# Performance work log

Measured on AMD Instinct MI355X. Metric: run time of the kernel, lower is better.

Reference implementation:

```python
import math
import jax, jax.numpy as jnp
import numpy as np

B, L, C, H = 8, 1024, 1024, 16
D = C // H  # head_dim = 64
MAX_SCALE_MUL = math.log(100.0)


def setup_inputs() -> dict:
    key = jax.random.key(0)
    ks = jax.random.split(key, 8)
    x = jax.random.normal(ks[0], (B, L, C), dtype=jnp.float32)
    # rotary frequencies: angle(l, j) = l * theta^(-2j/D), stored as (cos, sin)
    theta = 10000.0
    inv_freq = theta ** (-jnp.arange(0, D, 2, dtype=jnp.float32) / D)  # [D/2]
    ang = jnp.arange(L, dtype=jnp.float32)[:, None] * inv_freq[None, :]  # [L, D/2]
    freqs_cis = jnp.stack([jnp.cos(ang), jnp.sin(ang)], axis=-1)  # [L, D/2, 2]
    attn_bias = jnp.zeros((1, 1, L, L), dtype=jnp.float32)
    W_qkv = jax.random.normal(ks[1], (3 * C, C), dtype=jnp.float32) * (1.0 / math.sqrt(C))
    q_bias = jnp.zeros((C,), dtype=jnp.float32)
    v_bias = jnp.zeros((C,), dtype=jnp.float32)
    scale_mul_log = jnp.full((1, H, 1, 1), math.log(4.0), dtype=jnp.float32)
    W_proj = jax.random.normal(ks[2], (C, C), dtype=jnp.float32) * (1.0 / math.sqrt(C))
    b_proj = jnp.zeros((C,), dtype=jnp.float32)
    return {"x": x, "freqs_cis": freqs_cis, "attn_bias": attn_bias,
            "W_qkv": W_qkv, "q_bias": q_bias, "v_bias": v_bias,
            "scale_mul_log": scale_mul_log, "W_proj": W_proj, "b_proj": b_proj}


def _l2norm(t):
    # F.normalize(t, dim=-1): t / max(||t||_2, eps)
    n = jnp.sqrt(jnp.sum(t * t, axis=-1, keepdims=True))
    return t / jnp.maximum(n, 1e-12)


def _rope(t, fr):
    # t: [B,H,L,D]; fr: [L,D/2,2] (cos,sin). Complex mul on adjacent pairs.
    b, h, l, d = t.shape
    t2 = t.reshape(b, h, l, d // 2, 2)
    c = fr[None, None, :, :, 0]
    s = fr[None, None, :, :, 1]
    re = t2[..., 0] * c - t2[..., 1] * s
    im = t2[..., 0] * s + t2[..., 1] * c
    return jnp.stack([re, im], axis=-1).reshape(b, h, l, d)


def reference(x, freqs_cis, attn_bias, W_qkv, q_bias, v_bias, scale_mul_log, W_proj, b_proj):
    b, l, c = x.shape
    bias = jnp.concatenate([q_bias, jnp.zeros_like(q_bias), v_bias])  # [3C]
    qkv = (x @ W_qkv.T + bias).reshape(b, l, 3, H, D)
    # permute(2,0,3,1,4) -> q,k,v each [B,H,L,D]
    q = jnp.transpose(qkv[:, :, 0], (0, 2, 1, 3))
    k = jnp.transpose(qkv[:, :, 1], (0, 2, 1, 3))
    v = jnp.transpose(qkv[:, :, 2], (0, 2, 1, 3))
    # attn_l2_norm path: learned per-head scale, softmax scale = 1
    scale_mul = jnp.exp(jnp.minimum(scale_mul_log, MAX_SCALE_MUL))  # [1,H,1,1]
    q = _l2norm(q) * scale_mul
    k = _l2norm(k)
    q = _rope(q, freqs_cis)
    k = _rope(k, freqs_cis)
    scores = jnp.einsum('bhqd,bhkd->bhqk', q, k) * 1.0 + attn_bias
    attn = jax.nn.softmax(scores, axis=-1)
    out = jnp.einsum('bhqk,bhkd->bhqd', attn, v)
    out = jnp.transpose(out, (0, 2, 1, 3)).reshape(b, l, c)
    return out @ W_proj.T + b_proj
```

## Files before the change

kernel.cpp:

```cpp
#include <hip/hip_runtime.h>
#include <math.h>
#include <type_traits>

#define PB 8
#define PL 1024
#define PC 1024
#define PH 16
#define PD 64
#define MAX_SCALE_MUL 4.605170185988092f
#define LOG2E 1.4426950408889634f

typedef __attribute__((ext_vector_type(8))) short s16x8;
typedef __attribute__((ext_vector_type(4))) float f32x4;

#define MFMA16(a, b, c) __builtin_amdgcn_mfma_f32_16x16x32_bf16(a, b, c, 0, 0, 0)

#if __has_builtin(__builtin_amdgcn_exp2f)
#define EXP2(x) __builtin_amdgcn_exp2f(x)
#else
#define EXP2(x) exp2f(x)
#endif

__device__ __forceinline__ unsigned short f2bf(float f) {
    unsigned u = __float_as_uint(f);
    unsigned r = (u + 0x7fffu + ((u >> 16) & 1u)) >> 16;
    return (unsigned short)r;
}

__device__ __forceinline__ unsigned pk2bf(float a, float b) {
#if __has_builtin(__builtin_amdgcn_cvt_pk_bf16_f32)
    typedef __attribute__((ext_vector_type(2))) __bf16 bf16x2_t;
    bf16x2_t r = __builtin_amdgcn_cvt_pk_bf16_f32(a, b);
    return __builtin_bit_cast(unsigned, r);
#else
    return (unsigned)f2bf(a) | ((unsigned)f2bf(b) << 16);
#endif
}

__device__ __forceinline__ void gl2lds16(const void* g, void* l) {
    __builtin_amdgcn_global_load_lds(
        (const __attribute__((address_space(1))) unsigned int*)g,
        (__attribute__((address_space(3))) unsigned int*)l, 16, 0, 0);
}

__global__ __launch_bounds__(256) void cast3f_kernel(
    const float* __restrict__ a, const float* __restrict__ b,
    const float* __restrict__ c, const float* __restrict__ bias,
    unsigned short* __restrict__ oa, unsigned short* __restrict__ ob,
    unsigned short* __restrict__ oc, int* __restrict__ flag)
{
    int blk = blockIdx.x;
    if (blk >= 12288) {
        int idx = (blk - 12288) * 256 + threadIdx.x;
        const float4* b4 = (const float4*)bias;
        bool nz = false;
#pragma unroll
        for (int i = 0; i < 4; i++) {
            float4 v = b4[idx * 4 + i];
            nz |= (v.x != 0.f) | (v.y != 0.f) | (v.z != 0.f) | (v.w != 0.f);
        }
        if (nz) atomicOr(flag, 1);
        return;
    }
    const float* src; unsigned short* dst; int base;
    if (blk < 8192)       { src = a; dst = oa; base = blk; }
    else if (blk < 11264) { src = b; dst = ob; base = blk - 8192; }
    else                  { src = c; dst = oc; base = blk - 11264; }
    int i = base * 256 + threadIdx.x;
    float4 v = ((const float4*)src)[i];
    ((uint2*)dst)[i] = make_uint2(pk2bf(v.x, v.y), pk2bf(v.z, v.w));
}

__global__ __launch_bounds__(256) void gemm_qkv_lean(
    const unsigned short* __restrict__ Xh,
    const unsigned short* __restrict__ Wh,
    const float* __restrict__ qb, const float* __restrict__ vb,
    const float* __restrict__ freqs,
    unsigned short* __restrict__ Qh, unsigned short* __restrict__ Kh,
    unsigned short* __restrict__ Vt)
{
    __shared__ unsigned short As[128 * 64];
    __shared__ unsigned short Bs[128 * 64];
    const int tid  = threadIdx.x;
    const int wave = tid >> 6, lane = tid & 63;
    const int wm = wave & 1, wn = wave >> 1;
    const int quad = lane >> 4, rr = lane & 15;
    const int m0 = blockIdx.x * 128;
    const int n0 = blockIdx.y * 128;
    const bool vmode = (n0 >= 2048);

    f32x4 acc[4][4];
#pragma unroll
    for (int i = 0; i < 4; i++)
#pragma unroll
        for (int j = 0; j < 4; j++) acc[i][j] = (f32x4){0.f, 0.f, 0.f, 0.f};

    const int r8 = lane >> 3;
    const int c8 = lane & 7;
    const int g  = c8 ^ r8;
    const unsigned short* gA = Xh + (size_t)(m0 + wave * 32 + r8) * 1024 + g * 8;
    const unsigned short* gB = Wh + (size_t)(n0 + wave * 32 + r8) * 1024 + g * 8;
    unsigned short* lA = &As[(wave * 32) * 64];
    unsigned short* lB = &Bs[(wave * 32) * 64];

    const int swz8 = rr & 7;

    auto kloop = [&](auto vm) {
        constexpr int VM = decltype(vm)::value;
        for (int k0 = 0; k0 < 16; k0++) {
#pragma unroll
            for (int t = 0; t < 4; t++) {
                gl2lds16(gA + (size_t)t * 8192, &lA[(t * 8) * 64]);
                gl2lds16(gB + (size_t)t * 8192, &lB[(t * 8) * 64]);
            }
            gA += 64; gB += 64;
            __syncthreads();

#pragma unroll
            for (int kk = 0; kk < 2; kk++) {
                const int coff = ((kk * 4 + quad) ^ swz8) * 8;
                s16x8 wf[4], xf[4];
#pragma unroll
                for (int i = 0; i < 4; i++)
                    wf[i] = *(const s16x8*)&Bs[(wn * 64 + i * 16 + rr) * 64 + coff];
#pragma unroll
                for (int j = 0; j < 4; j++)
                    xf[j] = *(const s16x8*)&As[(wm * 64 + j * 16 + rr) * 64 + coff];
                if constexpr (VM == 0) {
#pragma unroll
                    for (int i = 0; i < 4; i++)
#pragma unroll
                        for (int j = 0; j < 4; j++)
                            acc[i][j] = MFMA16(wf[i], xf[j], acc[i][j]);
                } else {
#pragma unroll
                    for (int i = 0; i < 4; i++)
#pragma unroll
                        for (int j = 0; j < 4; j++)
                            acc[i][j] = MFMA16(xf[j], wf[i], acc[i][j]);
                }
            }
            __syncthreads();
        }
    };
    if (vmode) kloop(std::integral_constant<int, 1>{});
    else       kloop(std::integral_constant<int, 0>{});

    const int b   = m0 >> 10;
    const int h   = ((n0 & 1023) + wn * 64) >> 6;
    const int lb0 = (m0 & 1023) + wm * 64;

    if (vmode) {
        unsigned short* basep = Vt + (size_t)(b * PH + h) * PD * PL;
#pragma unroll
        for (int i = 0; i < 4; i++) {
            const int d = i * 16 + rr;
            const float bv = vb[h * 64 + d];
#pragma unroll
            for (int j = 0; j < 4; j++) {
                const int l0 = lb0 + j * 16 + quad * 4;
                uint2 pk = make_uint2(pk2bf(acc[i][j][0] + bv, acc[i][j][1] + bv),
                                      pk2bf(acc[i][j][2] + bv, acc[i][j][3] + bv));
                *(uint2*)(basep + (size_t)d * PL + l0) = pk;
            }
        }
    } else {
        const int which = n0 >> 10;
        if (which == 0) {
            unsigned short* basep = Qh + (size_t)(b * PH + h) * PL * PD;
#pragma unroll
            for (int i = 0; i < 4; i++) {
                const int d0 = i * 16 + quad * 4;
                const float4 b4 = *(const float4*)(qb + h * 64 + d0);
#pragma unroll
                for (int j = 0; j < 4; j++) {
                    const int l = lb0 + j * 16 + rr;
                    uint2 pk = make_uint2(
                        pk2bf(acc[i][j][0] + b4.x, acc[i][j][1] + b4.y),
                        pk2bf(acc[i][j][2] + b4.z, acc[i][j][3] + b4.w));
                    *(uint2*)(basep + (size_t)l * PD + d0) = pk;
                }
            }
        } else {
            unsigned short* basep = Kh + (size_t)(b * PH + h) * PL * PD;
            const float2* fr2 = (const float2*)freqs;
#pragma unroll
            for (int j = 0; j < 4; j++) {
                float ss = 0.f;
#pragma unroll
                for (int i = 0; i < 4; i++)
                    ss = fmaf(acc[i][j][0], acc[i][j][0],
                         fmaf(acc[i][j][1], acc[i][j][1],
                         fmaf(acc[i][j][2], acc[i][j][2],
                         fmaf(acc[i][j][3], acc[i][j][3], ss))));
                ss += __shfl_xor(ss, 16);
                ss += __shfl_xor(ss, 32);
                const float scale = 1.0f / fmaxf(sqrtf(ss), 1e-12f);
                const int l = lb0 + j * 16 + rr;
#pragma unroll
                for (int i = 0; i < 4; i++) {
                    const int d0 = i * 16 + quad * 4;
                    const float2 cs0 = fr2[(size_t)l * 32 + (d0 >> 1)];
                    const float2 cs1 = fr2[(size_t)l * 32 + (d0 >> 1) + 1];
                    const float a0 = acc[i][j][0] * scale, a1 = acc[i][j][1] * scale;
                    const float a2 = acc[i][j][2] * scale, a3 = acc[i][j][3] * scale;
                    uint2 pk = make_uint2(
                        pk2bf(a0 * cs0.x - a1 * cs0.y, fmaf(a0, cs0.y, a1 * cs0.x)),
                        pk2bf(a2 * cs1.x - a3 * cs1.y, fmaf(a2, cs1.y, a3 * cs1.x)));
                    *(uint2*)(basep + (size_t)l * PD + d0) = pk;
                }
            }
        }
    }
}

__global__ __launch_bounds__(256, 4) void attn_mfma(
    const unsigned short* __restrict__ Qh, const unsigned short* __restrict__ Kh,
    const unsigned short* __restrict__ Vt, const float* __restrict__ bias,
    const float* __restrict__ sml, const int* __restrict__ biasflag,
    const float* __restrict__ freqs, unsigned short* __restrict__ O)
{
    __shared__ unsigned short Ks[2][64 * 64];
    __shared__ unsigned short Vs[2][64 * 64];
    __shared__ unsigned int   Ps[4][16 * 32];

    const int tid  = threadIdx.x;
    const int wave = tid >> 6, lane = tid & 63;
    const int quad = lane >> 4, rr = lane & 15;
    const int bh = blockIdx.x, q0 = blockIdx.y * 128;
    const int b = bh >> 4, h = bh & 15;
    const int hasbias = *biasflag;

    const float M = __expf(fminf(sml[h], MAX_SCALE_MUL)) * LOG2E;
    const f32x4 negM = (f32x4){-M, -M, -M, -M};

    const int sr = wave * 16 + (lane >> 3);
    const int sc = lane & 7;
    const int sg = sc ^ (sr & 7);
    const int swz8 = rr & 7;
    const int psw  = (rr & 7) << 2;

    const size_t kvbase = (size_t)bh * PL * PD;
    const float2* fr2 = (const float2*)freqs;

    auto stage = [&](int buf, int kb) {
        gl2lds16(Kh + kvbase + (size_t)(kb * 64 + sr) * PD + sg * 8,
                 &Ks[buf][(wave * 16) * 64]);
        gl2lds16(Kh + kvbase + (size_t)(kb * 64 + sr + 8) * PD + sg * 8,
                 &Ks[buf][(wave * 16 + 8) * 64]);
        gl2lds16(Vt + kvbase + (size_t)sr * PL + kb * 64 + sg * 8,
                 &Vs[buf][(wave * 16) * 64]);
        gl2lds16(Vt + kvbase + (size_t)(sr + 8) * PL + kb * 64 + sg * 8,
                 &Vs[buf][(wave * 16 + 8) * 64]);
    };

    stage(0, 0);

    s16x8 qB[2][2];
#pragma unroll
    for (int g = 0; g < 2; g++) {
        const int ql = q0 + g * 64 + wave * 16 + rr;
        const size_t qoff = ((size_t)bh * PL + ql) * PD;
        uint4 r0 = *(const uint4*)(Qh + qoff + quad * 8);
        uint4 r1 = *(const uint4*)(Qh + qoff + 32 + quad * 8);
        unsigned uu[8] = {r0.x, r0.y, r0.z, r0.w, r1.x, r1.y, r1.z, r1.w};
        float ss = 0.f;
#pragma unroll
        for (int m = 0; m < 8; m++) {
            float lo = __uint_as_float(uu[m] << 16);
            float hi = __uint_as_float(uu[m] & 0xffff0000u);
            ss = fmaf(lo, lo, fmaf(hi, hi, ss));
        }
        ss += __shfl_xor(ss, 16);
        ss += __shfl_xor(ss, 32);
        const float scale = M / fmaxf(sqrtf(ss), 1e-12f);
        unsigned outw[8];
#pragma unroll
        for (int m = 0; m < 8; m++) {
            const int idx = (m >> 2) * 16 + quad * 4 + (m & 3);
            float2 cs = fr2[(size_t)ql * 32 + idx];
            float lo = __uint_as_float(uu[m] << 16);
            float hi = __uint_as_float(uu[m] & 0xffff0000u);
            float av = lo * scale, bv = hi * scale;
            outw[m] = pk2bf(av * cs.x - bv * cs.y, fmaf(av, cs.y, bv * cs.x));
        }
        qB[g][0] = __builtin_bit_cast(s16x8, make_uint4(outw[0], outw[1], outw[2], outw[3]));
        qB[g][1] = __builtin_bit_cast(s16x8, make_uint4(outw[4], outw[5], outw[6], outw[7]));
    }

    f32x4 accO[2][4];
#pragma unroll
    for (int g = 0; g < 2; g++)
#pragma unroll
        for (int jd = 0; jd < 4; jd++) accO[g][jd] = (f32x4){0.f, 0.f, 0.f, 0.f};
    float lsum[2] = {0.f, 0.f};

    __syncthreads();

    auto kbloop = [&](auto hb) {
        constexpr int HB = decltype(hb)::value;
        int cur = 0;
        for (int kb = 0; kb < 16; kb++) {
            if (kb < 15) stage(cur ^ 1, kb + 1);

            unsigned ps[2][4][2];
#pragma unroll
            for (int s = 0; s < 4; s++) {
                const s16x8 k0 = *(const s16x8*)&Ks[cur][(s * 16 + rr) * 64 + ((0 + quad) ^ swz8) * 8];
                const s16x8 k1 = *(const s16x8*)&Ks[cur][(s * 16 + rr) * 64 + ((4 + quad) ^ swz8) * 8];
#pragma unroll
                for (int g = 0; g < 2; g++) {
                    __builtin_amdgcn_s_setprio(1);
                    f32x4 z = MFMA16(k0, qB[g][0], negM);
                    z = MFMA16(k1, qB[g][1], z);
                    __builtin_amdgcn_s_setprio(0);
                    if constexpr (HB) {
                        const float* brow = bias + (size_t)(q0 + g * 64 + wave * 16 + rr) * PL + kb * 64;
                        float4 bv = *(const float4*)(brow + s * 16 + quad * 4);
                        z[0] = fmaf(bv.x, LOG2E, z[0]);
                        z[1] = fmaf(bv.y, LOG2E, z[1]);
                        z[2] = fmaf(bv.z, LOG2E, z[2]);
                        z[3] = fmaf(bv.w, LOG2E, z[3]);
                    }
                    z[0] = EXP2(z[0]); z[1] = EXP2(z[1]);
                    z[2] = EXP2(z[2]); z[3] = EXP2(z[3]);
                    lsum[g] += (z[0] + z[1]) + (z[2] + z[3]);
                    ps[g][s][0] = pk2bf(z[0], z[1]);
                    ps[g][s][1] = pk2bf(z[2], z[3]);
                }
            }

            s16x8 pB[2][2];
#pragma unroll
            for (int g = 0; g < 2; g++) {
#pragma unroll
                for (int s = 0; s < 4; s++)
                    *(uint2*)&Ps[wave][rr * 32 + ((s * 8 + quad * 2) ^ psw)] =
                        make_uint2(ps[g][s][0], ps[g][s][1]);
                pB[g][0] = *(const s16x8*)&Ps[wave][rr * 32 + ((quad * 4) ^ psw)];
                pB[g][1] = *(const s16x8*)&Ps[wave][rr * 32 + ((16 + quad * 4) ^ psw)];
            }
#pragma unroll
            for (int jd = 0; jd < 4; jd++) {
                const s16x8 v0 = *(const s16x8*)&Vs[cur][(jd * 16 + rr) * 64 + ((0 + quad) ^ swz8) * 8];
                const s16x8 v1 = *(const s16x8*)&Vs[cur][(jd * 16 + rr) * 64 + ((4 + quad) ^ swz8) * 8];
                __builtin_amdgcn_s_setprio(1);
#pragma unroll
                for (int g = 0; g < 2; g++) {
                    accO[g][jd] = MFMA16(v0, pB[g][0], accO[g][jd]);
                    accO[g][jd] = MFMA16(v1, pB[g][1], accO[g][jd]);
                }
                __builtin_amdgcn_s_setprio(0);
            }

            __syncthreads();
            cur ^= 1;
        }
    };
    if (hasbias) kbloop(std::integral_constant<int, 1>{});
    else         kbloop(std::integral_constant<int, 0>{});

    const int lr = lane >> 2, cch = lane & 3;
    const int pswl = (lr & 7) << 2;
#pragma unroll
    for (int g = 0; g < 2; g++) {
        float ls = lsum[g];
        ls += __shfl_xor(ls, 16);
        ls += __shfl_xor(ls, 32);
        float inv = 1.0f / ls;
#pragma unroll
        for (int jd = 0; jd < 4; jd++) {
            *(uint2*)&Ps[wave][rr * 32 + ((jd * 8 + quad * 2) ^ psw)] =
                make_uint2(pk2bf(accO[g][jd][0] * inv, accO[g][jd][1] * inv),
                           pk2bf(accO[g][jd][2] * inv, accO[g][jd][3] * inv));
        }
        uint4 w0 = *(const uint4*)&Ps[wave][lr * 32 + ((cch * 8) ^ pswl)];
        uint4 w1 = *(const uint4*)&Ps[wave][lr * 32 + ((cch * 8 + 4) ^ pswl)];
        size_t ob = ((size_t)(b * PL + q0 + g * 64 + wave * 16 + lr) * PC + h * PD);
        *(uint4*)(O + ob + cch * 16)     = w0;
        *(uint4*)(O + ob + cch * 16 + 8) = w1;
    }
}

__global__ __launch_bounds__(256) void gemm_proj_mfma(
    const unsigned short* __restrict__ Ah,
    const unsigned short* __restrict__ Wh,
    const float* __restrict__ bp, float* __restrict__ Out)
{
    __shared__ unsigned short As[128 * 64];
    __shared__ unsigned short Bs[128 * 64];
    const int tid  = threadIdx.x;
    const int wave = tid >> 6, lane = tid & 63;
    const int wm = wave & 1, wn = wave >> 1;
    const int quad = lane >> 4, rr = lane & 15;
    const int m0 = blockIdx.x * 128, n0 = blockIdx.y * 128;

    f32x4 acc[4][4];
#pragma unroll
    for (int i = 0; i < 4; i++)
#pragma unroll
        for (int j = 0; j < 4; j++) acc[i][j] = (f32x4){0.f, 0.f, 0.f, 0.f};

    const int r8 = lane >> 3;
    const int c8 = lane & 7;
    const int g  = c8 ^ r8;
    const unsigned short* gA = Ah + (size_t)(m0 + wave * 32 + r8) * 1024 + g * 8;
    const unsigned short* gB = Wh + (size_t)(n0 + wave * 32 + r8) * 1024 + g * 8;
    unsigned short* lA = &As[(wave * 32) * 64];
    unsigned short* lB = &Bs[(wave * 32) * 64];

    const int swz8 = rr & 7;

    for (int k0 = 0; k0 < 16; k0++) {
#pragma unroll
        for (int t = 0; t < 4; t++) {
            gl2lds16(gA + (size_t)t * 8192, &lA[(t * 8) * 64]);
            gl2lds16(gB + (size_t)t * 8192, &lB[(t * 8) * 64]);
        }
        gA += 64; gB += 64;
        __syncthreads();

#pragma unroll
        for (int kk = 0; kk < 2; kk++) {
            const int coff = ((kk * 4 + quad) ^ swz8) * 8;
            s16x8 wf[4], xf[4];
#pragma unroll
            for (int i = 0; i < 4; i++)
                wf[i] = *(const s16x8*)&Bs[(wn * 64 + i * 16 + rr) * 64 + coff];
#pragma unroll
            for (int j = 0; j < 4; j++)
                xf[j] = *(const s16x8*)&As[(wm * 64 + j * 16 + rr) * 64 + coff];
#pragma unroll
            for (int i = 0; i < 4; i++)
#pragma unroll
                for (int j = 0; j < 4; j++)
                    acc[i][j] = MFMA16(wf[i], xf[j], acc[i][j]);
        }
        __syncthreads();
    }

#pragma unroll
    for (int i = 0; i < 4; i++) {
        const int nn = n0 + wn * 64 + i * 16 + quad * 4;
        const float4 bb = *(const float4*)(bp + nn);
#pragma unroll
        for (int j = 0; j < 4; j++) {
            const int m = m0 + wm * 64 + j * 16 + rr;
            float4 o = make_float4(acc[i][j][0] + bb.x, acc[i][j][1] + bb.y,
                                   acc[i][j][2] + bb.z, acc[i][j][3] + bb.w);
            *(float4*)(Out + (size_t)m * 1024 + nn) = o;
        }
    }
}

extern "C" void kernel_launch(void* const* d_in, const int* in_sizes, int n_in,
                              void* d_out, int out_size, void* d_ws, size_t ws_size,
                              hipStream_t stream)
{
    const float* x         = (const float*)d_in[0];
    const float* freqs     = (const float*)d_in[1];
    const float* attn_bias = (const float*)d_in[2];
    const float* W_qkv     = (const float*)d_in[3];
    const float* q_bias    = (const float*)d_in[4];
    const float* v_bias    = (const float*)d_in[5];
    const float* sml       = (const float*)d_in[6];
    const float* W_proj    = (const float*)d_in[7];
    const float* b_proj    = (const float*)d_in[8];
    float* out = (float*)d_out;

    unsigned char* w = (unsigned char*)d_ws;
    const size_t MB = 1ull << 20;
    unsigned short* xh  = (unsigned short*)(w + 0);
    unsigned short* wqh = (unsigned short*)(w + 16 * MB);
    unsigned short* wph = (unsigned short*)(w + 22 * MB);
    unsigned short* Qh  = (unsigned short*)(w + 24 * MB);
    unsigned short* Kh  = (unsigned short*)(w + 40 * MB);
    unsigned short* Vt  = (unsigned short*)(w + 72 * MB);
    unsigned short* Oh  = (unsigned short*)(w + 88 * MB);
    int*            flg = (int*)(w + 104 * MB);

    hipMemsetAsync(flg, 0, sizeof(int), stream);
    cast3f_kernel<<<12544, 256, 0, stream>>>(x, W_qkv, W_proj, attn_bias,
                                             xh, wqh, wph, flg);
    gemm_qkv_lean<<<dim3(64, 24), 256, 0, stream>>>(
        xh, wqh, q_bias, v_bias, freqs, Qh, Kh, Vt);
    attn_mfma<<<dim3(128, 8), 256, 0, stream>>>(Qh, Kh, Vt, attn_bias, sml, flg, freqs, Oh);
    gemm_proj_mfma<<<dim3(64, 8), 256, 0, stream>>>(Oh, wph, b_proj, out);
}
```

Before: 250.9 us.

## Double-buffer QKV GEMM LDS tiles and shrink N tile to 64

```diff
diff --git a/kernel.cpp b/kernel.cpp
--- a/kernel.cpp
+++ b/kernel.cpp
@@ -71,7 +71,7 @@
     ((uint2*)dst)[i] = make_uint2(pk2bf(v.x, v.y), pk2bf(v.z, v.w));
 }
 
-__global__ __launch_bounds__(256) void gemm_qkv_lean(
+__global__ __launch_bounds__(256, 4) void gemm_qkv_lean(
     const unsigned short* __restrict__ Xh,
     const unsigned short* __restrict__ Wh,
     const float* __restrict__ qb, const float* __restrict__ vb,
@@ -79,76 +79,80 @@
     unsigned short* __restrict__ Qh, unsigned short* __restrict__ Kh,
     unsigned short* __restrict__ Vt)
 {
-    __shared__ unsigned short As[128 * 64];
-    __shared__ unsigned short Bs[128 * 64];
+    __shared__ unsigned short As[2][128 * 64];
+    __shared__ unsigned short Bs[2][64 * 64];
     const int tid  = threadIdx.x;
     const int wave = tid >> 6, lane = tid & 63;
-    const int wm = wave & 1, wn = wave >> 1;
     const int quad = lane >> 4, rr = lane & 15;
     const int m0 = blockIdx.x * 128;
-    const int n0 = blockIdx.y * 128;
+    const int n0 = blockIdx.y * 64;
     const bool vmode = (n0 >= 2048);
 
-    f32x4 acc[4][4];
+    f32x4 acc[4][2];
 #pragma unroll
     for (int i = 0; i < 4; i++)
 #pragma unroll
-        for (int j = 0; j < 4; j++) acc[i][j] = (f32x4){0.f, 0.f, 0.f, 0.f};
+        for (int j = 0; j < 2; j++) acc[i][j] = (f32x4){0.f, 0.f, 0.f, 0.f};
 
     const int r8 = lane >> 3;
     const int c8 = lane & 7;
     const int g  = c8 ^ r8;
     const unsigned short* gA = Xh + (size_t)(m0 + wave * 32 + r8) * 1024 + g * 8;
-    const unsigned short* gB = Wh + (size_t)(n0 + wave * 32 + r8) * 1024 + g * 8;
-    unsigned short* lA = &As[(wave * 32) * 64];
-    unsigned short* lB = &Bs[(wave * 32) * 64];
+    const unsigned short* gB = Wh + (size_t)(n0 + wave * 16 + r8) * 1024 + g * 8;
 
     const int swz8 = rr & 7;
+
+    auto stageAB = [&](int buf, int k0) {
+        const size_t co = (size_t)k0 * 64;
+#pragma unroll
+        for (int t = 0; t < 4; t++)
+            gl2lds16(gA + co + (size_t)t * 8192, &As[buf][(wave * 32 + t * 8) * 64]);
+#pragma unroll
+        for (int t = 0; t < 2; t++)
+            gl2lds16(gB + co + (size_t)t * 8192, &Bs[buf][(wave * 16 + t * 8) * 64]);
+    };
 
     auto kloop = [&](auto vm) {
         constexpr int VM = decltype(vm)::value;
+        stageAB(0, 0);
+        __syncthreads();
+        int cur = 0;
         for (int k0 = 0; k0 < 16; k0++) {
-#pragma unroll
-            for (int t = 0; t < 4; t++) {
-                gl2lds16(gA + (size_t)t * 8192, &lA[(t * 8) * 64]);
-                gl2lds16(gB + (size_t)t * 8192, &lB[(t * 8) * 64]);
-            }
-            gA += 64; gB += 64;
-            __syncthreads();
-
+            if (k0 < 15) stageAB(cur ^ 1, k0 + 1);
 #pragma unroll
             for (int kk = 0; kk < 2; kk++) {
                 const int coff = ((kk * 4 + quad) ^ swz8) * 8;
-                s16x8 wf[4], xf[4];
+                s16x8 wf[4], xf[2];
 #pragma unroll
                 for (int i = 0; i < 4; i++)
-                    wf[i] = *(const s16x8*)&Bs[(wn * 64 + i * 16 + rr) * 64 + coff];
-#pragma unroll
-                for (int j = 0; j < 4; j++)
-                    xf[j] = *(const s16x8*)&As[(wm * 64 + j * 16 + rr) * 64 + coff];
+                    wf[i] = *(const s16x8*)&Bs[cur][(i * 16 + rr) * 64 + coff];
+#pragma unroll
+                for (int j = 0; j < 2; j++)
+                    xf[j] = *(const s16x8*)&As[cur][(wave * 32 + j * 16 + rr) * 64 + coff];
                 if constexpr (VM == 0) {
 #pragma unroll
                     for (int i = 0; i < 4; i++)
 #pragma unroll
-                        for (int j = 0; j < 4; j++)
+                        for (int j = 0; j < 2; j++)
                             acc[i][j] = MFMA16(wf[i], xf[j], acc[i][j]);
                 } else {
 #pragma unroll
                     for (int i = 0; i < 4; i++)
 #pragma unroll
-                        for (int j = 0; j < 4; j++)
+                        for (int j = 0; j < 2; j++)
                             acc[i][j] = MFMA16(xf[j], wf[i], acc[i][j]);
                 }
             }
             __syncthreads();
+            cur ^= 1;
         }
     };
     if (vmode) kloop(std::integral_constant<int, 1>{});
     else       kloop(std::integral_constant<int, 0>{});
 
     const int b   = m0 >> 10;
-    const int h   = ((n0 & 1023) + wn * 64) >> 6;
-    const int lb0 = (m0 & 1023) + wm * 64;
+    const int h   = (n0 >> 6) & 15;
+    const int lb0 = (m0 & 1023) + wave * 32;
 
     if (vmode) {
         unsigned short* basep = Vt + (size_t)(b * PH + h) * PD * PL;
@@ -157,7 +161,7 @@
             const int d = i * 16 + rr;
             const float bv = vb[h * 64 + d];
 #pragma unroll
-            for (int j = 0; j < 4; j++) {
+            for (int j = 0; j < 2; j++) {
                 const int l0 = lb0 + j * 16 + quad * 4;
                 uint2 pk = make_uint2(pk2bf(acc[i][j][0] + bv, acc[i][j][1] + bv),
                                       pk2bf(acc[i][j][2] + bv, acc[i][j][3] + bv));
@@ -173,7 +177,7 @@
                 const int d0 = i * 16 + quad * 4;
                 const float4 b4 = *(const float4*)(qb + h * 64 + d0);
 #pragma unroll
-                for (int j = 0; j < 4; j++) {
+                for (int j = 0; j < 2; j++) {
                     const int l = lb0 + j * 16 + rr;
                     uint2 pk = make_uint2(
                         pk2bf(acc[i][j][0] + b4.x, acc[i][j][1] + b4.y),
@@ -185,7 +189,7 @@
             unsigned short* basep = Kh + (size_t)(b * PH + h) * PL * PD;
             const float2* fr2 = (const float2*)freqs;
 #pragma unroll
-            for (int j = 0; j < 4; j++) {
+            for (int j = 0; j < 2; j++) {
                 float ss = 0.f;
 #pragma unroll
                 for (int i = 0; i < 4; i++)
@@ -482,7 +486,7 @@
     hipMemsetAsync(flg, 0, sizeof(int), stream);
     cast3f_kernel<<<12544, 256, 0, stream>>>(x, W_qkv, W_proj, attn_bias,
                                              xh, wqh, wph, flg);
-    gemm_qkv_lean<<<dim3(64, 24), 256, 0, stream>>>(
+    gemm_qkv_lean<<<dim3(64, 48), 256, 0, stream>>>(
         xh, wqh, q_bias, v_bias, freqs, Qh, Kh, Vt);
     attn_mfma<<<dim3(128, 8), 256, 0, stream>>>(Qh, Kh, Vt, attn_bias, sml, flg, freqs, Oh);
     gemm_proj_mfma<<<dim3(64, 8), 256, 0, stream>>>(Oh, wph, b_proj, out);
```

Measured after the change: 260.6 us. 3.9% more time.
